# Optimization experiments

Measured on AMD Instinct MI355X. Metric: run time of the kernel, lower is better.

Reference implementation:

```python
import jax, jax.numpy as jnp
import numpy as np

D_OUT = 1024

def setup_inputs() -> dict:
    key = jax.random.key(0)
    k1, k2, k3, k4 = jax.random.split(key, 4)
    x = jax.random.normal(k1, (4, 2048, 1024), dtype=jnp.float32)
    # torch.nn.Linear weights are [d_out, d_in]
    s = 1.0 / np.sqrt(1024)
    W_q = jax.random.uniform(k2, (D_OUT, 1024), dtype=jnp.float32, minval=-s, maxval=s)
    W_k = jax.random.uniform(k3, (D_OUT, 1024), dtype=jnp.float32, minval=-s, maxval=s)
    W_v = jax.random.uniform(k4, (D_OUT, 1024), dtype=jnp.float32, minval=-s, maxval=s)
    return {"x": x, "W_q": W_q, "W_k": W_k, "W_v": W_v}

def reference(x, W_q, W_k, W_v):
    b, n, d_in = x.shape
    q = jnp.einsum('bnd,od->bno', x, W_q)  # [b, n, d_out]
    k = jnp.einsum('bnd,od->bno', x, W_k)
    v = jnp.einsum('bnd,od->bno', x, W_v)
    scores = jnp.einsum('bqd,bkd->bqk', q, k)  # full N x N score matrix
    causal = jnp.tril(jnp.ones((n, n), dtype=bool))
    scores = jnp.where(causal, scores, -jnp.inf)
    weights = jax.nn.softmax(scores / jnp.sqrt(jnp.float32(D_OUT)), axis=-1)
    # dropout p=0.0 -> identity (eval)
    return jnp.einsum('bqk,bkd->bqd', weights, v)
```

## Files before the change

### kernel.cpp

```cpp
#include <hip/hip_runtime.h>
#include <hip/hip_bf16.h>
#include <stdint.h>

typedef unsigned short ushort_t;
typedef __attribute__((ext_vector_type(4))) float f32x4;
typedef __attribute__((ext_vector_type(8))) __bf16 bf16x8;
typedef __attribute__((ext_vector_type(8))) unsigned short ushort8;
typedef __attribute__((ext_vector_type(4))) unsigned short ushort4v;

__device__ __forceinline__ float bf2f(ushort_t u) {
  union { unsigned u32; float f; } x; x.u32 = ((unsigned)u) << 16; return x.f;
}
__device__ __forceinline__ ushort_t f2bf(float f) {
  union { float f; unsigned u; } x; x.f = f;
  unsigned r = x.u + 0x7FFF + ((x.u >> 16) & 1);
  return (ushort_t)(r >> 16);
}

__device__ __forceinline__ void gld16(const ushort_t* g, ushort_t* l) {
  __builtin_amdgcn_global_load_lds(
      (const __attribute__((address_space(1))) uint32_t*)g,
      (__attribute__((address_space(3))) uint32_t*)l, 16, 0, 0);
}

__global__ __launch_bounds__(256) void cast_all_kernel(
    const float* __restrict__ x, const float* __restrict__ wq,
    const float* __restrict__ wk, const float* __restrict__ wv,
    ushort_t* __restrict__ xb, ushort_t* __restrict__ wqb,
    ushort_t* __restrict__ wkb, ushort_t* __restrict__ wvb,
    float* __restrict__ rowsum) {
  int blk = blockIdx.x;
  if (blk >= 4096 + 1536) {
    int idx = (blk - (4096 + 1536)) * 256 + threadIdx.x;
    f32x4 z = {0.f, 0.f, 0.f, 0.f};
    ((f32x4*)rowsum)[idx * 2] = z;
    ((f32x4*)rowsum)[idx * 2 + 1] = z;
    return;
  }
  const float* in;
  ushort_t* out;
  int i;
  if (blk < 4096) {
    in = x; out = xb; i = blk * 256 + threadIdx.x;
  } else {
    int w = (blk - 4096) >> 9;
    int lb = (blk - 4096) & 511;
    in = (w == 0) ? wq : (w == 1) ? wk : wv;
    out = (w == 0) ? wqb : (w == 1) ? wkb : wvb;
    i = lb * 256 + threadIdx.x;
  }
  const f32x4* p = (const f32x4*)in;
  f32x4 a = p[2 * i];
  f32x4 b = p[2 * i + 1];
  ushort8 o;
  o[0] = f2bf(a[0]); o[1] = f2bf(a[1]); o[2] = f2bf(a[2]); o[3] = f2bf(a[3]);
  o[4] = f2bf(b[0]); o[5] = f2bf(b[1]); o[6] = f2bf(b[2]); o[7] = f2bf(b[3]);
  *((ushort8*)out + i) = o;
}

enum { OUT_EXP = 0, OUT_F32N = 2 };

__device__ __forceinline__ void gemm8_core(
    const ushort_t* __restrict__ A, const ushort_t* __restrict__ B, int Kd,
    int kEnd, int m0, int n0,
    ushort_t* a0, ushort_t* a1, ushort_t* a2,
    ushort_t* b0, ushort_t* b1, ushort_t* b2,
    f32x4 (&acc)[4][4]) {
  int tid = threadIdx.x;
  int lane = tid & 63;
  int wave = tid >> 6;
  int wm = wave >> 1;
  int wn = wave & 1;
  int ln15 = lane & 15;
  int kq = lane >> 4;
  int xk = ln15 & 7;

  int rowc = tid >> 3;
  int ksw = ((tid & 7) ^ (rowc & 7)) * 8;
  const ushort_t* aB = A + (size_t)(m0 + rowc) * Kd + ksw;
  const ushort_t* bB = B + (size_t)(n0 + rowc) * Kd + ksw;

  const int nt = kEnd >> 6;

  ushort_t *pAr = a0, *pAn = a1, *pAw = a2;
  ushort_t *pBr = b0, *pBn = b1, *pBw = b2;

#pragma unroll
  for (int c = 0; c < 4; ++c)
    gld16(aB + (size_t)(64 * c) * Kd, a0 + (size_t)(tid + 512 * c) * 8);
#pragma unroll
  for (int c = 0; c < 2; ++c)
    gld16(bB + (size_t)(64 * c) * Kd, b0 + (size_t)(tid + 512 * c) * 8);
#pragma unroll
  for (int c = 0; c < 4; ++c)
    gld16(aB + (size_t)(64 * c) * Kd + 64, a1 + (size_t)(tid + 512 * c) * 8);
#pragma unroll
  for (int c = 0; c < 2; ++c)
    gld16(bB + (size_t)(64 * c) * Kd + 64, b1 + (size_t)(tid + 512 * c) * 8);
  asm volatile("s_waitcnt vmcnt(6)" ::: "memory");
  __builtin_amdgcn_s_barrier();

  bf16x8 bfr[2][4];
  for (int t = 0; t < nt; ++t) {
    const bool st = (t + 2) < nt;
    const int k2 = (t + 2) << 6;
    bf16x8 af[2][2];
#pragma unroll
    for (int il = 0; il < 2; ++il) {
      int ro = (wm * 64 + il * 16 + ln15) * 64;
#pragma unroll
      for (int s = 0; s < 2; ++s)
        af[s][il] = *(const bf16x8*)&pAr[ro + (((s * 4 + kq) ^ xk) * 8)];
    }
#pragma unroll
    for (int j = 0; j < 4; ++j) {
      int ro = (wn * 64 + j * 16 + ln15) * 64;
#pragma unroll
      for (int s = 0; s < 2; ++s)
        bfr[s][j] = *(const bf16x8*)&pBr[ro + (((s * 4 + kq) ^ xk) * 8)];
    }
    if (st) {
      gld16(aB + (size_t)0 * Kd + k2, pAw + (size_t)tid * 8);
      gld16(aB + (size_t)64 * Kd + k2, pAw + (size_t)(tid + 512) * 8);
      gld16(bB + k2, pBw + (size_t)tid * 8);
    }
    __builtin_amdgcn_s_barrier();
    asm volatile("s_waitcnt lgkmcnt(0)" ::: "memory");
    __builtin_amdgcn_sched_barrier(0);
    __builtin_amdgcn_s_setprio(1);
#pragma unroll
    for (int s = 0; s < 2; ++s)
#pragma unroll
      for (int il = 0; il < 2; ++il)
#pragma unroll
        for (int j = 0; j < 4; ++j)
          acc[il][j] = __builtin_amdgcn_mfma_f32_16x16x32_bf16(
              af[s][il], bfr[s][j], acc[il][j], 0, 0, 0);
    __builtin_amdgcn_s_setprio(0);
    __builtin_amdgcn_s_barrier();
#pragma unroll
    for (int il = 0; il < 2; ++il) {
      int ro = (wm * 64 + (il + 2) * 16 + ln15) * 64;
#pragma unroll
      for (int s = 0; s < 2; ++s)
        af[s][il] = *(const bf16x8*)&pAr[ro + (((s * 4 + kq) ^ xk) * 8)];
    }
    if (st) {
      gld16(aB + (size_t)128 * Kd + k2, pAw + (size_t)(tid + 1024) * 8);
      gld16(aB + (size_t)192 * Kd + k2, pAw + (size_t)(tid + 1536) * 8);
      gld16(bB + (size_t)64 * Kd + k2, pBw + (size_t)(tid + 512) * 8);
      asm volatile("s_waitcnt vmcnt(6)" ::: "memory");
    } else {
      asm volatile("s_waitcnt vmcnt(0)" ::: "memory");
    }
    __builtin_amdgcn_s_barrier();
    asm volatile("s_waitcnt lgkmcnt(0)" ::: "memory");
    __builtin_amdgcn_sched_barrier(0);
    __builtin_amdgcn_s_setprio(1);
#pragma unroll
    for (int s = 0; s < 2; ++s)
#pragma unroll
      for (int il = 0; il < 2; ++il)
#pragma unroll
        for (int j = 0; j < 4; ++j)
          acc[il + 2][j] = __builtin_amdgcn_mfma_f32_16x16x32_bf16(
              af[s][il], bfr[s][j], acc[il + 2][j], 0, 0, 0);
    __builtin_amdgcn_s_setprio(0);
    __builtin_amdgcn_s_barrier();
    ushort_t* tA = pAr; pAr = pAn; pAn = pAw; pAw = tA;
    ushort_t* tB = pBr; pBr = pBn; pBn = pBw; pBw = tB;
  }
}

__global__ __launch_bounds__(512, 2) void gemm_qkv8(
    const ushort_t* __restrict__ xb, const ushort_t* __restrict__ wq,
    const ushort_t* __restrict__ wk, const ushort_t* __restrict__ wv,
    ushort_t* __restrict__ Qb, ushort_t* __restrict__ Kb,
    ushort_t* __restrict__ Vt) {
  int m0 = blockIdx.x * 256, n0 = blockIdx.y * 128;
  int z = blockIdx.z;
  const ushort_t* B = (z == 0) ? wq : (z == 1) ? wk : wv;

  __shared__ ushort_t As[3][256 * 64];
  __shared__ ushort_t Bs[3][128 * 64];

  f32x4 acc[4][4];
#pragma unroll
  for (int i = 0; i < 4; ++i)
#pragma unroll
    for (int j = 0; j < 4; ++j) acc[i][j] = f32x4{0.f, 0.f, 0.f, 0.f};

  gemm8_core(xb, B, 1024, 1024, m0, n0, As[0], As[1], As[2], Bs[0], Bs[1],
             Bs[2], acc);

  int tid = threadIdx.x;
  int lane = tid & 63;
  int wave = tid >> 6;
  int wm = wave >> 1, wn = wave & 1;
  int ln15 = lane & 15, kq = lane >> 4;

  if (z < 2) {
    ushort_t* C = (z == 0) ? Qb : Kb;
#pragma unroll
    for (int i = 0; i < 4; ++i) {
      int row0 = m0 + wm * 64 + i * 16 + kq * 4;
#pragma unroll
      for (int j = 0; j < 4; ++j) {
        int col = n0 + wn * 64 + j * 16 + ln15;
#pragma unroll
        for (int r = 0; r < 4; ++r)
          C[(size_t)(row0 + r) * 1024 + col] = f2bf(acc[i][j][r]);
      }
    }
  } else {
#pragma unroll
    for (int i = 0; i < 4; ++i) {
      int gm = m0 + wm * 64 + i * 16 + kq * 4;
      int b = gm >> 11, nn = gm & 2047;
#pragma unroll
      for (int j = 0; j < 4; ++j) {
        int d = n0 + wn * 64 + j * 16 + ln15;
        ushort4v v;
#pragma unroll
        for (int r = 0; r < 4; ++r) v[r] = f2bf(acc[i][j][r]);
        *(ushort4v*)&Vt[(size_t)b * (2048 * 1024) + (size_t)d * 2048 + nn] = v;
      }
    }
  }
}

template <int OUT, bool CAUSAL_SKIP, bool K_LIMIT>
__global__ __launch_bounds__(512, 2) void gemm8k(
    const ushort_t* __restrict__ Ag, const ushort_t* __restrict__ Bg,
    void* __restrict__ Cg, int N, int Kd,
    long sA, long sB, long sC, float scale, float* __restrict__ rowsum) {
  int m0 = blockIdx.x * 256, n0 = blockIdx.y * 128;
  if (CAUSAL_SKIP && n0 > m0 + 255) return;
  int bz = blockIdx.z;
  const ushort_t* A = Ag + (size_t)bz * sA;
  const ushort_t* B = Bg + (size_t)bz * sB;
  int kEnd = K_LIMIT ? min(Kd, m0 + 256) : Kd;

  __shared__ ushort_t As[3][256 * 64];
  __shared__ ushort_t Bs[3][128 * 64];

  f32x4 acc[4][4];
#pragma unroll
  for (int i = 0; i < 4; ++i)
#pragma unroll
    for (int j = 0; j < 4; ++j) acc[i][j] = f32x4{0.f, 0.f, 0.f, 0.f};

  gemm8_core(A, B, Kd, kEnd, m0, n0, As[0], As[1], As[2], Bs[0], Bs[1], Bs[2],
             acc);

  int tid = threadIdx.x;
  int lane = tid & 63;
  int wave = tid >> 6;
  int wm = wave >> 1, wn = wave & 1;
  int ln15 = lane & 15, kq = lane >> 4;

  if (OUT == OUT_EXP) {
    ushort_t* C = (ushort_t*)Cg + (size_t)bz * sC;
    float* rs = rowsum + (size_t)bz * 2048;
#pragma unroll
    for (int i = 0; i < 4; ++i) {
      int row0 = m0 + wm * 64 + i * 16 + kq * 4;
#pragma unroll
      for (int r = 0; r < 4; ++r) {
        int grow = row0 + r;
        float psum = 0.f;
#pragma unroll
        for (int j = 0; j < 4; ++j) {
          int col = n0 + wn * 64 + j * 16 + ln15;
          float e = (col <= grow) ? __expf(acc[i][j][r] * scale) : 0.f;
          C[(size_t)grow * N + col] = f2bf(e);
          psum += e;
        }
        psum += __shfl_xor(psum, 1);
        psum += __shfl_xor(psum, 2);
        psum += __shfl_xor(psum, 4);
        psum += __shfl_xor(psum, 8);
        if (ln15 == 0) atomicAdd(&rs[grow], psum);
      }
    }
  } else {
    float* C = (float*)Cg + (size_t)bz * sC;
    const float* rs = rowsum + (size_t)bz * 2048;
#pragma unroll
    for (int i = 0; i < 4; ++i) {
      int row0 = m0 + wm * 64 + i * 16 + kq * 4;
#pragma unroll
      for (int r = 0; r < 4; ++r) {
        float inv = 1.0f / rs[row0 + r];
#pragma unroll
        for (int j = 0; j < 4; ++j) {
          int col = n0 + wn * 64 + j * 16 + ln15;
          C[(size_t)(row0 + r) * N + col] = acc[i][j][r] * inv;
        }
      }
    }
  }
}

extern "C" void kernel_launch(void* const* d_in, const int* in_sizes, int n_in,
                              void* d_out, int out_size, void* d_ws, size_t ws_size,
                              hipStream_t stream) {
  const float* x = (const float*)d_in[0];
  const float* Wq = (const float*)d_in[1];
  const float* Wk = (const float*)d_in[2];
  const float* Wv = (const float*)d_in[3];
  float* out = (float*)d_out;
  char* ws = (char*)d_ws;

  ushort_t* xb = (ushort_t*)(ws);
  ushort_t* wqb = (ushort_t*)(ws + (16ull << 20));
  ushort_t* wkb = (ushort_t*)(ws + (18ull << 20));
  ushort_t* wvb = (ushort_t*)(ws + (20ull << 20));
  ushort_t* Qb = (ushort_t*)(ws + (22ull << 20));
  ushort_t* Kb = (ushort_t*)(ws + (38ull << 20));
  ushort_t* Vt = (ushort_t*)(ws + (54ull << 20));
  ushort_t* Eb = (ushort_t*)(ws + (70ull << 20));
  float* rowsum = (float*)(ws + (102ull << 20));

  cast_all_kernel<<<4096 + 3 * 512 + 4, 256, 0, stream>>>(
      x, Wq, Wk, Wv, xb, wqb, wkb, wvb, rowsum);

  dim3 gQKV(8192 / 256, 1024 / 128, 3);
  gemm_qkv8<<<gQKV, 512, 0, stream>>>(xb, wqb, wkb, wvb, Qb, Kb, Vt);

  dim3 gS(2048 / 256, 2048 / 128, 4);
  gemm8k<OUT_EXP, true, false><<<gS, 512, 0, stream>>>(
      Qb, Kb, Eb, 2048, 1024, 2048 * 1024, 2048 * 1024, 2048 * 2048,
      0.03125f, rowsum);

  dim3 gO(2048 / 256, 1024 / 128, 4);
  gemm8k<OUT_F32N, false, true><<<gO, 512, 0, stream>>>(
      Eb, Vt, out, 1024, 2048, 2048 * 2048, 1024 * 2048, 2048 * 1024,
      1.0f, rowsum);
}
```

Before: 239.3 us.

## Use 128x128 single-buffered GEMM with split-K atomics for attention stages

```diff
diff --git a/kernel.cpp b/kernel.cpp
--- a/kernel.cpp
+++ b/kernel.cpp
@@ -28,11 +28,17 @@
     const float* __restrict__ wk, const float* __restrict__ wv,
     ushort_t* __restrict__ xb, ushort_t* __restrict__ wqb,
     ushort_t* __restrict__ wkb, ushort_t* __restrict__ wvb,
-    float* __restrict__ rowsum) {
+    float* __restrict__ rowsum, float* __restrict__ outz) {
   int blk = blockIdx.x;
+  f32x4 z = {0.f, 0.f, 0.f, 0.f};
+  if (blk >= 4096 + 1536 + 4) {
+    int idx = (blk - (4096 + 1536 + 4)) * 256 + threadIdx.x;
+    ((f32x4*)outz)[idx * 2] = z;
+    ((f32x4*)outz)[idx * 2 + 1] = z;
+    return;
+  }
   if (blk >= 4096 + 1536) {
     int idx = (blk - (4096 + 1536)) * 256 + threadIdx.x;
-    f32x4 z = {0.f, 0.f, 0.f, 0.f};
     ((f32x4*)rowsum)[idx * 2] = z;
     ((f32x4*)rowsum)[idx * 2 + 1] = z;
     return;
@@ -58,7 +64,147 @@
   *((ushort8*)out + i) = o;
 }
 
+#define BM 128
+#define BN 128
+#define BK 64
+
 enum { OUT_EXP = 0, OUT_F32N = 2 };
+
+__device__ __forceinline__ void gemm_core(
+    const ushort_t* __restrict__ A, const ushort_t* __restrict__ B, int Kd,
+    int kBeg, int kEnd, int m0, int n0, ushort_t* As, ushort_t* Bs,
+    f32x4 (&acc)[4][4]) {
+  int tid = threadIdx.x;
+  int lane = tid & 63;
+  int wave = tid >> 6;
+  int wr = (wave >> 1) * 64;
+  int wc = (wave & 1) * 64;
+  int ln15 = lane & 15;
+  int kq = lane >> 4;
+
+  int row = tid >> 3;
+  int ksw = ((tid & 7) ^ (row & 7)) * 8;
+  const ushort_t* aB = A + (size_t)(m0 + row) * Kd + ksw;
+  const ushort_t* bB = B + (size_t)(n0 + row) * Kd + ksw;
+  int xk = ln15 & 7;
+
+  for (int k0 = kBeg; k0 < kEnd; k0 += BK) {
+    __syncthreads();
+#pragma unroll
+    for (int r = 0; r < 4; ++r) {
+      gld16(aB + (size_t)(32 * r) * Kd + k0, &As[(tid + 256 * r) * 8]);
+      gld16(bB + (size_t)(32 * r) * Kd + k0, &Bs[(tid + 256 * r) * 8]);
+    }
+    __syncthreads();
+#pragma unroll
+    for (int s = 0; s < 2; ++s) {
+      bf16x8 af[4], bfr[4];
+#pragma unroll
+      for (int i = 0; i < 4; ++i)
+        af[i] = *(const bf16x8*)
+            &As[(wr + i * 16 + ln15) * BK + (((s * 4 + kq) ^ xk) * 8)];
+#pragma unroll
+      for (int j = 0; j < 4; ++j)
+        bfr[j] = *(const bf16x8*)
+            &Bs[(wc + j * 16 + ln15) * BK + (((s * 4 + kq) ^ xk) * 8)];
+#pragma unroll
+      for (int i = 0; i < 4; ++i)
+#pragma unroll
+        for (int j = 0; j < 4; ++j)
+          acc[i][j] = __builtin_amdgcn_mfma_f32_16x16x32_bf16(
+              af[i], bfr[j], acc[i][j], 0, 0, 0);
+    }
+  }
+}
+
+template <int OUT, bool CAUSAL_SKIP, bool K_LIMIT, bool KCHUNK>
+__global__ __launch_bounds__(256, 3) void gemm_bt(
+    const ushort_t* __restrict__ Ag, const ushort_t* __restrict__ Bg,
+    void* __restrict__ Cg, int N, int Kd,
+    long sA, long sB, long sC, float scale, float* __restrict__ rowsum) {
+  int m0 = blockIdx.x * BM, n0 = blockIdx.y * BN;
+  if (CAUSAL_SKIP && n0 > m0 + (BM - 1)) return;
+  int bz, kBeg = 0, kEnd;
+  if (KCHUNK) {
+    bz = blockIdx.z >> 1;
+    int kf = K_LIMIT ? min(Kd, m0 + BM) : Kd;
+    if (blockIdx.z & 1) {
+      if (kf <= 1024) return;
+      kBeg = 1024; kEnd = kf;
+    } else {
+      kEnd = min(kf, 1024);
+    }
+  } else {
+    bz = blockIdx.z;
+    kEnd = K_LIMIT ? min(Kd, m0 + BM) : Kd;
+  }
+  const ushort_t* A = Ag + (size_t)bz * sA;
+  const ushort_t* B = Bg + (size_t)bz * sB;
+
+  __shared__ ushort_t As[BM * BK];
+  __shared__ ushort_t Bs[BN * BK];
+
+  f32x4 acc[4][4];
+#pragma unroll
+  for (int i = 0; i < 4; ++i)
+#pragma unroll
+    for (int j = 0; j < 4; ++j) acc[i][j] = f32x4{0.f, 0.f, 0.f, 0.f};
+
+  gemm_core(A, B, Kd, kBeg, kEnd, m0, n0, As, Bs, acc);
+
+  int tid = threadIdx.x;
+  int lane = tid & 63;
+  int wave = tid >> 6;
+  int wr = (wave >> 1) * 64;
+  int wc = (wave & 1) * 64;
+  int ln15 = lane & 15;
+  int kq = lane >> 4;
+
+  if (OUT == OUT_EXP) {
+    ushort_t* C = (ushort_t*)Cg + (size_t)bz * sC;
+    float* rs = rowsum + (size_t)bz * 2048;
+#pragma unroll
+    for (int i = 0; i < 4; ++i) {
+      int row0 = m0 + wr + i * 16 + kq * 4;
+#pragma unroll
+      for (int r = 0; r < 4; ++r) {
+        int grow = row0 + r;
+        float psum = 0.f;
+#pragma unroll
+        for (int j = 0; j < 4; ++j) {
+          int col = n0 + wc + j * 16 + ln15;
+          float e = (col <= grow) ? __expf(acc[i][j][r] * scale) : 0.f;
+          C[(size_t)grow * N + col] = f2bf(e);
+          psum += e;
+        }
+        psum += __shfl_xor(psum, 1);
+        psum += __shfl_xor(psum, 2);
+        psum += __shfl_xor(psum, 4);
+        psum += __shfl_xor(psum, 8);
+        if (ln15 == 0) atomicAdd(&rs[grow], psum);
+      }
+    }
+  } else {
+    float* C = (float*)Cg + (size_t)bz * sC;
+    const float* rs = rowsum + (size_t)bz * 2048;
+#pragma unroll
+    for (int i = 0; i < 4; ++i) {
+      int row0 = m0 + wr + i * 16 + kq * 4;
+#pragma unroll
+      for (int r = 0; r < 4; ++r) {
+        float inv = 1.0f / rs[row0 + r];
+#pragma unroll
+        for (int j = 0; j < 4; ++j) {
+          int col = n0 + wc + j * 16 + ln15;
+          if (KCHUNK)
+            atomicAdd(&C[(size_t)(row0 + r) * N + col], acc[i][j][r] * inv);
+          else
+            C[(size_t)(row0 + r) * N + col] = acc[i][j][r] * inv;
+        }
+      }
+    }
+  }
+}
 
 __device__ __forceinline__ void gemm8_core(
     const ushort_t* __restrict__ A, const ushort_t* __restrict__ B, int Kd,
@@ -100,55 +246,49 @@
   asm volatile("s_waitcnt vmcnt(6)" ::: "memory");
   __builtin_amdgcn_s_barrier();
 
-  bf16x8 bfr[2][4];
   for (int t = 0; t < nt; ++t) {
     const bool st = (t + 2) < nt;
     const int k2 = (t + 2) << 6;
-    bf16x8 af[2][2];
-#pragma unroll
-    for (int il = 0; il < 2; ++il) {
-      int ro = (wm * 64 + il * 16 + ln15) * 64;
-#pragma unroll
-      for (int s = 0; s < 2; ++s)
-        af[s][il] = *(const bf16x8*)&pAr[ro + (((s * 4 + kq) ^ xk) * 8)];
-    }
-#pragma unroll
-    for (int j = 0; j < 4; ++j) {
-      int ro = (wn * 64 + j * 16 + ln15) * 64;
-#pragma unroll
-      for (int s = 0; s < 2; ++s)
-        bfr[s][j] = *(const bf16x8*)&pBr[ro + (((s * 4 + kq) ^ xk) * 8)];
-    }
+    const ushort_t* aT = aB + k2;
+    const ushort_t* bT = bB + k2;
+    bf16x8 af[4], bf[4];
+#pragma unroll
+    for (int il = 0; il < 4; ++il)
+      af[il] = *(const bf16x8*)
+          &pAr[(wm * 64 + il * 16 + ln15) * 64 + ((kq ^ xk) * 8)];
+#pragma unroll
+    for (int j = 0; j < 4; ++j)
+      bf[j] = *(const bf16x8*)
+          &pBr[(wn * 64 + j * 16 + ln15) * 64 + ((kq ^ xk) * 8)];
     if (st) {
-      gld16(aB + (size_t)0 * Kd + k2, pAw + (size_t)tid * 8);
-      gld16(aB + (size_t)64 * Kd + k2, pAw + (size_t)(tid + 512) * 8);
-      gld16(bB + k2, pBw + (size_t)tid * 8);
+      gld16(aT, pAw + (size_t)tid * 8);
+      gld16(aT + (size_t)64 * Kd, pAw + (size_t)(tid + 512) * 8);
+      gld16(bT, pBw + (size_t)tid * 8);
     }
     __builtin_amdgcn_s_barrier();
     asm volatile("s_waitcnt lgkmcnt(0)" ::: "memory");
     __builtin_amdgcn_sched_barrier(0);
     __builtin_amdgcn_s_setprio(1);
 #pragma unroll
-    for (int s = 0; s < 2; ++s)
-#pragma unroll
-      for (int il = 0; il < 2; ++il)
-#pragma unroll
-        for (int j = 0; j < 4; ++j)
-          acc[il][j] = __builtin_amdgcn_mfma_f32_16x16x32_bf16(
-              af[s][il], bfr[s][j], acc[il][j], 0, 0, 0);
+    for (int il = 0; il < 4; ++il)
+#pragma unroll
+      for (int j = 0; j < 4; ++j)
+        acc[il][j] = __builtin_amdgcn_mfma_f32_16x16x32_bf16(
+            af[il], bf[j], acc[il][j], 0, 0, 0);
     __builtin_amdgcn_s_setprio(0);
     __builtin_amdgcn_s_barrier();
 #pragma unroll
-    for (int il = 0; il < 2; ++il) {
-      int ro = (wm * 64 + (il + 2) * 16 + ln15) * 64;
-#pragma unroll
-      for (int s = 0; s < 2; ++s)
-        af[s][il] = *(const bf16x8*)&pAr[ro + (((s * 4 + kq) ^ xk) * 8)];
-    }
+    for (int il = 0; il < 4; ++il)
+      af[il] = *(const bf16x8*)
+          &pAr[(wm * 64 + il * 16 + ln15) * 64 + (((4 + kq) ^ xk) * 8)];
+#pragma unroll
+    for (int j = 0; j < 4; ++j)
+      bf[j] = *(const bf16x8*)
+          &pBr[(wn * 64 + j * 16 + ln15) * 64 + (((4 + kq) ^ xk) * 8)];
     if (st) {
-      gld16(aB + (size_t)128 * Kd + k2, pAw + (size_t)(tid + 1024) * 8);
-      gld16(aB + (size_t)192 * Kd + k2, pAw + (size_t)(tid + 1536) * 8);
-      gld16(bB + (size_t)64 * Kd + k2, pBw + (size_t)(tid + 512) * 8);
+      gld16(aT + (size_t)128 * Kd, pAw + (size_t)(tid + 1024) * 8);
+      gld16(aT + (size_t)192 * Kd, pAw + (size_t)(tid + 1536) * 8);
+      gld16(bT + (size_t)64 * Kd, pBw + (size_t)(tid + 512) * 8);
       asm volatile("s_waitcnt vmcnt(6)" ::: "memory");
     } else {
       asm volatile("s_waitcnt vmcnt(0)" ::: "memory");
@@ -158,13 +298,11 @@
     __builtin_amdgcn_sched_barrier(0);
     __builtin_amdgcn_s_setprio(1);
 #pragma unroll
-    for (int s = 0; s < 2; ++s)
-#pragma unroll
-      for (int il = 0; il < 2; ++il)
-#pragma unroll
-        for (int j = 0; j < 4; ++j)
-          acc[il + 2][j] = __builtin_amdgcn_mfma_f32_16x16x32_bf16(
-              af[s][il], bfr[s][j], acc[il + 2][j], 0, 0, 0);
+    for (int il = 0; il < 4; ++il)
+#pragma unroll
+      for (int j = 0; j < 4; ++j)
+        acc[il][j] = __builtin_amdgcn_mfma_f32_16x16x32_bf16(
+            af[il], bf[j], acc[il][j], 0, 0, 0);
     __builtin_amdgcn_s_setprio(0);
     __builtin_amdgcn_s_barrier();
     ushort_t* tA = pAr; pAr = pAn; pAn = pAw; pAw = tA;
@@ -224,79 +362,6 @@
 #pragma unroll
         for (int r = 0; r < 4; ++r) v[r] = f2bf(acc[i][j][r]);
         *(ushort4v*)&Vt[(size_t)b * (2048 * 1024) + (size_t)d * 2048 + nn] = v;
-      }
-    }
-  }
-}
-
-template <int OUT, bool CAUSAL_SKIP, bool K_LIMIT>
-__global__ __launch_bounds__(512, 2) void gemm8k(
-    const ushort_t* __restrict__ Ag, const ushort_t* __restrict__ Bg,
-    void* __restrict__ Cg, int N, int Kd,
-    long sA, long sB, long sC, float scale, float* __restrict__ rowsum) {
-  int m0 = blockIdx.x * 256, n0 = blockIdx.y * 128;
-  if (CAUSAL_SKIP && n0 > m0 + 255) return;
-  int bz = blockIdx.z;
-  const ushort_t* A = Ag + (size_t)bz * sA;
-  const ushort_t* B = Bg + (size_t)bz * sB;
-  int kEnd = K_LIMIT ? min(Kd, m0 + 256) : Kd;
-
-  __shared__ ushort_t As[3][256 * 64];
-  __shared__ ushort_t Bs[3][128 * 64];
-
-  f32x4 acc[4][4];
-#pragma unroll
-  for (int i = 0; i < 4; ++i)
-#pragma unroll
-    for (int j = 0; j < 4; ++j) acc[i][j] = f32x4{0.f, 0.f, 0.f, 0.f};
-
-  gemm8_core(A, B, Kd, kEnd, m0, n0, As[0], As[1], As[2], Bs[0], Bs[1], Bs[2],
-             acc);
-
-  int tid = threadIdx.x;
-  int lane = tid & 63;
-  int wave = tid >> 6;
-  int wm = wave >> 1, wn = wave & 1;
-  int ln15 = lane & 15, kq = lane >> 4;
-
-  if (OUT == OUT_EXP) {
-    ushort_t* C = (ushort_t*)Cg + (size_t)bz * sC;
-    float* rs = rowsum + (size_t)bz * 2048;
-#pragma unroll
-    for (int i = 0; i < 4; ++i) {
-      int row0 = m0 + wm * 64 + i * 16 + kq * 4;
-#pragma unroll
-      for (int r = 0; r < 4; ++r) {
-        int grow = row0 + r;
-        float psum = 0.f;
-#pragma unroll
-        for (int j = 0; j < 4; ++j) {
-          int col = n0 + wn * 64 + j * 16 + ln15;
-          float e = (col <= grow) ? __expf(acc[i][j][r] * scale) : 0.f;
-          C[(size_t)grow * N + col] = f2bf(e);
-          psum += e;
-        }
-        psum += __shfl_xor(psum, 1);
-        psum += __shfl_xor(psum, 2);
-        psum += __shfl_xor(psum, 4);
-        psum += __shfl_xor(psum, 8);
-        if (ln15 == 0) atomicAdd(&rs[grow], psum);
-      }
-    }
-  } else {
-    float* C = (float*)Cg + (size_t)bz * sC;
-    const float* rs = rowsum + (size_t)bz * 2048;
-#pragma unroll
-    for (int i = 0; i < 4; ++i) {
-      int row0 = m0 + wm * 64 + i * 16 + kq * 4;
-#pragma unroll
-      for (int r = 0; r < 4; ++r) {
-        float inv = 1.0f / rs[row0 + r];
-#pragma unroll
-        for (int j = 0; j < 4; ++j) {
-          int col = n0 + wn * 64 + j * 16 + ln15;
-          C[(size_t)(row0 + r) * N + col] = acc[i][j][r] * inv;
-        }
       }
     }
   }
@@ -322,19 +387,19 @@
   ushort_t* Eb = (ushort_t*)(ws + (70ull << 20));
   float* rowsum = (float*)(ws + (102ull << 20));
 
-  cast_all_kernel<<<4096 + 3 * 512 + 4, 256, 0, stream>>>(
-      x, Wq, Wk, Wv, xb, wqb, wkb, wvb, rowsum);
+  cast_all_kernel<<<4096 + 3 * 512 + 4 + 4096, 256, 0, stream>>>(
+      x, Wq, Wk, Wv, xb, wqb, wkb, wvb, rowsum, out);
 
   dim3 gQKV(8192 / 256, 1024 / 128, 3);
   gemm_qkv8<<<gQKV, 512, 0, stream>>>(xb, wqb, wkb, wvb, Qb, Kb, Vt);
 
-  dim3 gS(2048 / 256, 2048 / 128, 4);
-  gemm8k<OUT_EXP, true, false><<<gS, 512, 0, stream>>>(
+  dim3 gS(2048 / BM, 2048 / BN, 4);
+  gemm_bt<OUT_EXP, true, false, false><<<gS, 256, 0, stream>>>(
       Qb, Kb, Eb, 2048, 1024, 2048 * 1024, 2048 * 1024, 2048 * 2048,
       0.03125f, rowsum);
 
-  dim3 gO(2048 / 256, 1024 / 128, 4);
-  gemm8k<OUT_F32N, false, true><<<gO, 512, 0, stream>>>(
+  dim3 gO(2048 / BM, 1024 / BN, 8);
+  gemm_bt<OUT_F32N, false, true, true><<<gO, 256, 0, stream>>>(
       Eb, Vt, out, 1024, 2048, 2048 * 2048, 1024 * 2048, 2048 * 1024,
       1.0f, rowsum);
 }
```

Result: slower. 251.2 us (+5.0%).
